# Optimization experiments

Hardware: AMD Instinct MI355X
Metric: run time of the kernel (lower is better)

Reference implementation:

```python
import jax, jax.numpy as jnp
import numpy as np

C_IN, SEQ_LEN, K, G = 12, 8192, 8, 64
DIVISOR = 2 if G > 1 else 1
_G = G // DIVISOR
MAX_EXP = int(np.log2((SEQ_LEN - 1) / (9 - 1)))
DILATIONS = [2 ** e for e in range(MAX_EXP + 1)]   # 10 dilations for seq_len=8192
PADDINGS = [(9 - 1) * d // 2 for d in DILATIONS]
C_IN_PER = int(np.clip(C_IN // 2, 2, 8))
BATCH = 32


def _normalize(W):
    # zero-mean, L1-normalized over the kernel taps (last dim)
    W = W - W.mean(-1, keepdims=True)
    return W / jnp.abs(W).sum(-1, keepdims=True)


def setup_inputs() -> dict:
    key = jax.random.key(0)
    kx, kw, ki = jax.random.split(key, 3)
    X = jax.random.normal(kx, (BATCH, C_IN, SEQ_LEN), dtype=jnp.float32)
    # W: (num_dilations, divisor, k*_g, 1, 9) grouped-conv kernels
    W = _normalize(jax.random.normal(kw, (len(DILATIONS), DIVISOR, K * _G, 1, 9), dtype=jnp.float32))
    # I: (num_dilations, divisor, _g, c_in_per) channel-gather indices
    I = jax.random.randint(ki, (len(DILATIONS), DIVISOR, _G, C_IN_PER), 0, C_IN)
    return {"X": X, "W": W, "I": I}


def _branch(inp, Wd, d, p):
    # inp: (bs, _G, L); Wd: (K*_G, 1, 9); grouped dilated conv, 1 in-ch -> K out-ch per group
    z = jax.lax.conv_general_dilated(
        inp, Wd, window_strides=(1,), padding=[(p, p)], rhs_dilation=(d,),
        dimension_numbers=("NCH", "OIH", "NCH"), feature_group_count=_G)
    bs = inp.shape[0]
    z = z.reshape(bs, _G, K, -1)                      # (bs, _G, K, L)
    max_vals = z.max(axis=2)                          # (bs, _G, L)
    max_idx = z.argmax(axis=2)
    min_idx = z.argmin(axis=2)
    # histogram over K bins: sum of max values at argmax bin; count at argmin bin
    cmax = jnp.stack([jnp.where(max_idx == i, max_vals, 0.0).sum(-1) for i in range(K)], axis=-1)
    cmin = jnp.stack([(min_idx == i).astype(inp.dtype).sum(-1) for i in range(K)], axis=-1)
    return cmax, cmin                                 # each (bs, _G, K)


def reference(X, W, I):
    diff_X = jnp.diff(X, axis=-1)
    Z = []
    for di, (d, p) in enumerate(zip(DILATIONS, PADDINGS)):
        for j in range(min(2, G)):
            src = X if j == 0 else diff_X
            inp = src[:, I[di, j]].sum(2)             # gather channels, sum -> (bs, _G, L)
            cmax, cmin = _branch(inp, W[di, j], d, p)
            Z.append(cmax)
            Z.append(cmin)
    Z = jnp.concatenate(Z, axis=1)                    # (bs, 4*num_dilations*_G, K)
    return jax.nn.relu(Z)
```

## Files before the change

kernel.cpp:

```cpp
#include <hip/hip_runtime.h>


typedef __fp16 h2_t __attribute__((ext_vector_type(2)));

#define NB    32
#define CIN   12
#define SEQ   8192
#define NG    32
#define CPER  6
#define OUTCH 1280
#define XS_FLOATS 7728
#define GRID  10240

template <int DI>
__device__ __forceinline__ void hydra_body(
    const float* __restrict__ X, const float* __restrict__ W,
    const int* __restrict__ I, float* __restrict__ out,
    float* Xs, float* Smx, int j, int b, int chunk) {

  constexpr int d   = 1 << DI;
  constexpr int R   = (d < 16) ? d : 16;
  constexpr int rb  = (DI < 4) ? DI : 4;
  constexpr int Mm  = SEQ / d;
  constexpr int TMc = 512 / R;
  constexpr int TM  = (TMc < Mm) ? TMc : Mm;
  constexpr int MC  = Mm / TM;
  constexpr int RC  = d / R;
  constexpr int NR  = (RC * MC) / 16;
  constexpr int SR  = TM + 8;
  constexpr int CS  = R * SR + 4;
  constexpr int CL  = (R >= 8) ? TM : (TM * R / 8);
  constexpr int REP = (R == 16) ? 2 : 1;

  const int L = SEQ - j;
  const int tid = threadIdx.x;
  const int g = tid >> 3, s = tid & 7;

  h2_t Wp[8][4];
  float Wt[8];
  {
    const float* wp = W + (size_t)((DI * 2 + j) * 256 + g * 8) * 9;
#pragma unroll
    for (int k = 0; k < 8; ++k) {
#pragma unroll
      for (int t = 0; t < 4; ++t)
        Wp[k][t] = __builtin_amdgcn_cvt_pkrtz(wp[k * 9 + 2 * t], wp[k * 9 + 2 * t + 1]);
      Wt[k] = wp[k * 9 + 8];
    }
  }
  const float* base[CPER];
  {
    const int* ip = I + ((DI * 2 + j) * NG + g) * CPER;
#pragma unroll
    for (int i = 0; i < CPER; ++i) base[i] = Xs + ip[i] * CS;
  }

#pragma unroll
  for (int k = 0; k < 8; ++k) Smx[k * 256 + tid] = 0.f;

  unsigned long long cmnp = 0ull;

  for (int n = 0; n < NR; ++n) {
    const int cidx = chunk + 16 * n;
    const int rc = cidx & (RC - 1);
    const int mc = cidx / RC;
    const int r0 = rc * R;
    const int m0 = mc * TM;

    if (NR > 1 && n) __syncthreads();

    {
      const float* xb0 = X + (size_t)b * CIN * SEQ;
      if (j == 0) {
        for (int f = tid; f < R * SR; f += 256) {
          int rr = f & (R - 1), mm = f >> rb, mp = m0 + mm - 4;
          int pos = r0 + rr + mp * d;
          bool ok = (mp >= 0) && (pos < L);
          int lo = rr * SR + mm;
          const float* xp = xb0 + pos;
#pragma unroll
          for (int ch = 0; ch < CIN; ++ch) {
            Xs[ch * CS + lo] = ok ? xp[0] : 0.f;
            xp += SEQ;
          }
        }
      } else {
        for (int f = tid; f < R * SR; f += 256) {
          int rr = f & (R - 1), mm = f >> rb, mp = m0 + mm - 4;
          int pos = r0 + rr + mp * d;
          bool ok = (mp >= 0) && (pos < L);
          int lo = rr * SR + mm;
          const float* xp = xb0 + pos;
#pragma unroll
          for (int ch = 0; ch < CIN; ++ch) {
            Xs[ch * CS + lo] = ok ? (xp[1] - xp[0]) : 0.f;
            xp += SEQ;
          }
        }
      }
    }
    __syncthreads();

#pragma unroll
    for (int rep = 0; rep < REP; ++rep) {
      int rr = (R == 16) ? (s + (rep << 3)) : (s & (R - 1));
      int mst = (R >= 8) ? 0 : ((s >> rb) * CL);
      int rowoff = rr * SR + mst;

      auto ldsum = [&](int idx) {
        float4 r = *reinterpret_cast<const float4*>(base[0] + idx);
#pragma unroll
        for (int i = 1; i < CPER; ++i) {
          float4 t = *reinterpret_cast<const float4*>(base[i] + idx);
          r.x += t.x; r.y += t.y; r.z += t.z; r.w += t.w;
        }
        return r;
      };

      float4 w0 = ldsum(rowoff);
      float4 w1 = ldsum(rowoff + 4);
#pragma unroll 1
      for (int st = 0; st < CL; st += 4) {
        float4 w2 = ldsum(rowoff + st + 8);
        float xv[12] = {w0.x, w0.y, w0.z, w0.w,
                        w1.x, w1.y, w1.z, w1.w,
                        w2.x, w2.y, w2.z, w2.w};
        h2_t E[5], O[5];
#pragma unroll
        for (int i = 0; i < 5; ++i) {
          E[i] = __builtin_amdgcn_cvt_pkrtz(xv[2 * i],     xv[2 * i + 1]);
          O[i] = __builtin_amdgcn_cvt_pkrtz(xv[2 * i + 1], xv[2 * i + 2]);
        }
#pragma unroll
        for (int p = 0; p < 4; ++p) {
          const h2_t* P = (p & 1) ? (O + (p >> 1)) : (E + (p >> 1));
          float tail = xv[8 + p];
          float zp[8];
#pragma unroll
          for (int k = 0; k < 8; ++k) {
            float acc = Wt[k] * tail;
            acc = __builtin_amdgcn_fdot2(Wp[k][3], P[3], acc, false);
            acc = __builtin_amdgcn_fdot2(Wp[k][2], P[2], acc, false);
            acc = __builtin_amdgcn_fdot2(Wp[k][1], P[1], acc, false);
            acc = __builtin_amdgcn_fdot2(Wp[k][0], P[0], acc, false);
            zp[k] = __uint_as_float((__float_as_uint(acc) & 0xFFFFFFF8u) | (unsigned)k);
          }
          float mxp = fmaxf(fmaxf(fmaxf(zp[0], zp[1]), fmaxf(zp[2], zp[3])),
                            fmaxf(fmaxf(zp[4], zp[5]), fmaxf(zp[6], zp[7])));
          float mnp = fminf(fminf(fminf(zp[0], zp[1]), fminf(zp[2], zp[3])),
                            fminf(fminf(zp[4], zp[5]), fminf(zp[6], zp[7])));
          unsigned mxb = __float_as_uint(mxp);
          Smx[((mxb & 7u) << 8) + tid] += mxp;
          unsigned mnb = __float_as_uint(mnp);
          cmnp += 1ull << ((mnb & 7u) << 3);
        }
        w0 = w1; w1 = w2;
      }
    }
  }

  __syncthreads();

  {
    int cbase = (DI * 2 + j) * 64;
    float sum = 0.f;
#pragma unroll
    for (int s2 = 0; s2 < 8; ++s2) sum += Smx[(s << 8) + (g << 3) + s2];
    atomicAdd(out + ((size_t)b * OUTCH + cbase + g) * 8 + s, sum);

    int cnts[8];
#pragma unroll
    for (int k = 0; k < 8; ++k) cnts[k] = (int)((cmnp >> (k * 8)) & 0xFFull);
#pragma unroll
    for (int k = 0; k < 8; ++k) {
#pragma unroll
      for (int off = 1; off < 8; off <<= 1)
        cnts[k] += __shfl_xor(cnts[k], off);
    }
    int vn = cnts[0];
#pragma unroll
    for (int k = 1; k < 8; ++k) vn = (s == k) ? cnts[k] : vn;
    atomicAdd(out + ((size_t)b * OUTCH + cbase + 32 + g) * 8 + s, (float)vn);
  }
}

__global__ __launch_bounds__(256, 3) void hydra_fused(
    const float* __restrict__ X, const float* __restrict__ W,
    const int* __restrict__ I, float* __restrict__ out) {
  __shared__ float Xs[XS_FLOATS];
  __shared__ float Smx[2048];
  int u = blockIdx.x;
  int dj = u % 20;
  int rest = u / 20;
  int b = rest & 31;
  int chunk = rest >> 5;
  int j = dj & 1;
  switch (dj >> 1) {
    case 0: hydra_body<0>(X, W, I, out, Xs, Smx, j, b, chunk); break;
    case 1: hydra_body<1>(X, W, I, out, Xs, Smx, j, b, chunk); break;
    case 2: hydra_body<2>(X, W, I, out, Xs, Smx, j, b, chunk); break;
    case 3: hydra_body<3>(X, W, I, out, Xs, Smx, j, b, chunk); break;
    case 4: hydra_body<4>(X, W, I, out, Xs, Smx, j, b, chunk); break;
    case 5: hydra_body<5>(X, W, I, out, Xs, Smx, j, b, chunk); break;
    case 6: hydra_body<6>(X, W, I, out, Xs, Smx, j, b, chunk); break;
    case 7: hydra_body<7>(X, W, I, out, Xs, Smx, j, b, chunk); break;
    case 8: hydra_body<8>(X, W, I, out, Xs, Smx, j, b, chunk); break;
    case 9: hydra_body<9>(X, W, I, out, Xs, Smx, j, b, chunk); break;
  }
}

__global__ void hydra_relu(float* __restrict__ out, int n) {
  int i = blockIdx.x * 256 + threadIdx.x;
  if (i < n) out[i] = fmaxf(out[i], 0.f);
}

extern "C" void kernel_launch(void* const* d_in, const int* in_sizes, int n_in,
                              void* d_out, int out_size, void* d_ws, size_t ws_size,
                              hipStream_t stream) {
  const float* X = (const float*)d_in[0];
  const float* W = (const float*)d_in[1];
  const int*   I = (const int*)d_in[2];
  float* out = (float*)d_out;

  (void)hipMemsetAsync(d_out, 0, (size_t)out_size * sizeof(float), stream);
  hydra_fused<<<GRID, 256, 0, stream>>>(X, W, I, out);
  hydra_relu<<<(out_size + 255) / 256, 256, 0, stream>>>(out, out_size);
}
```

Baseline: 428.3 us.

## Stage inputs as fp16 in LDS and sum channels with packed half adds

Result: slower. 453.9 us (+6.0%).

```diff
diff --git a/kernel.cpp b/kernel.cpp
--- a/kernel.cpp
+++ b/kernel.cpp
@@ -2,6 +2,7 @@
 
 
 typedef __fp16 h2_t __attribute__((ext_vector_type(2)));
+typedef _Float16 f16x8 __attribute__((ext_vector_type(8)));
 
 #define NB    32
 #define CIN   12
@@ -9,14 +10,14 @@
 #define NG    32
 #define CPER  6
 #define OUTCH 1280
-#define XS_FLOATS 7728
+#define XS_HALVES 9312
 #define GRID  10240
 
 template <int DI>
 __device__ __forceinline__ void hydra_body(
     const float* __restrict__ X, const float* __restrict__ W,
     const int* __restrict__ I, float* __restrict__ out,
-    float* Xs, float* Smx, int j, int b, int chunk) {
+    _Float16* Xs, float* Smx, int j, int b, int chunk) {
 
   constexpr int d   = 1 << DI;
   constexpr int R   = (d < 16) ? d : 16;
@@ -27,8 +28,8 @@
   constexpr int MC  = Mm / TM;
   constexpr int RC  = d / R;
   constexpr int NR  = (RC * MC) / 16;
-  constexpr int SR  = TM + 8;
-  constexpr int CS  = R * SR + 4;
+  constexpr int SR  = TM + 16;
+  constexpr int CS  = R * SR + 8;
   constexpr int CL  = (R >= 8) ? TM : (TM * R / 8);
   constexpr int REP = (R == 16) ? 2 : 1;
 
@@ -36,8 +37,7 @@
   const int tid = threadIdx.x;
   const int g = tid >> 3, s = tid & 7;
 
-  h2_t Wp[8][4];
-  float Wt[8];
+  h2_t Wp[8][5];
   {
     const float* wp = W + (size_t)((DI * 2 + j) * 256 + g * 8) * 9;
 #pragma unroll
@@ -45,10 +45,10 @@
 #pragma unroll
       for (int t = 0; t < 4; ++t)
         Wp[k][t] = __builtin_amdgcn_cvt_pkrtz(wp[k * 9 + 2 * t], wp[k * 9 + 2 * t + 1]);
-      Wt[k] = wp[k * 9 + 8];
-    }
-  }
-  const float* base[CPER];
+      Wp[k][4] = __builtin_amdgcn_cvt_pkrtz(wp[k * 9 + 8], 0.f);
+    }
+  }
+  const _Float16* base[CPER];
   {
     const int* ip = I + ((DI * 2 + j) * NG + g) * CPER;
 #pragma unroll
@@ -75,12 +75,12 @@
         for (int f = tid; f < R * SR; f += 256) {
           int rr = f & (R - 1), mm = f >> rb, mp = m0 + mm - 4;
           int pos = r0 + rr + mp * d;
-          bool ok = (mp >= 0) && (pos < L);
+          bool ok = (mp >= 0) && (mm < TM + 8) && (pos < L);
           int lo = rr * SR + mm;
           const float* xp = xb0 + pos;
 #pragma unroll
           for (int ch = 0; ch < CIN; ++ch) {
-            Xs[ch * CS + lo] = ok ? xp[0] : 0.f;
+            Xs[ch * CS + lo] = ok ? (_Float16)xp[0] : (_Float16)0.f;
             xp += SEQ;
           }
         }
@@ -88,12 +88,12 @@
         for (int f = tid; f < R * SR; f += 256) {
           int rr = f & (R - 1), mm = f >> rb, mp = m0 + mm - 4;
           int pos = r0 + rr + mp * d;
-          bool ok = (mp >= 0) && (pos < L);
+          bool ok = (mp >= 0) && (mm < TM + 8) && (pos < L);
           int lo = rr * SR + mm;
           const float* xp = xb0 + pos;
 #pragma unroll
           for (int ch = 0; ch < CIN; ++ch) {
-            Xs[ch * CS + lo] = ok ? (xp[1] - xp[0]) : 0.f;
+            Xs[ch * CS + lo] = ok ? (_Float16)(xp[1] - xp[0]) : (_Float16)0.f;
             xp += SEQ;
           }
         }
@@ -107,42 +107,50 @@
       int mst = (R >= 8) ? 0 : ((s >> rb) * CL);
       int rowoff = rr * SR + mst;
 
-      auto ldsum = [&](int idx) {
-        float4 r = *reinterpret_cast<const float4*>(base[0] + idx);
-#pragma unroll
-        for (int i = 1; i < CPER; ++i) {
-          float4 t = *reinterpret_cast<const float4*>(base[i] + idx);
-          r.x += t.x; r.y += t.y; r.z += t.z; r.w += t.w;
-        }
+      auto sum8 = [&](int idx) {
+        f16x8 r = *reinterpret_cast<const f16x8*>(base[0] + idx);
+#pragma unroll
+        for (int i = 1; i < CPER; ++i)
+          r = r + *reinterpret_cast<const f16x8*>(base[i] + idx);
         return r;
       };
 
-      float4 w0 = ldsum(rowoff);
-      float4 w1 = ldsum(rowoff + 4);
+      f16x8 a = sum8(rowoff);
+      f16x8 bw = sum8(rowoff + 8);
 #pragma unroll 1
-      for (int st = 0; st < CL; st += 4) {
-        float4 w2 = ldsum(rowoff + st + 8);
-        float xv[12] = {w0.x, w0.y, w0.z, w0.w,
-                        w1.x, w1.y, w1.z, w1.w,
-                        w2.x, w2.y, w2.z, w2.w};
-        h2_t E[5], O[5];
-#pragma unroll
-        for (int i = 0; i < 5; ++i) {
-          E[i] = __builtin_amdgcn_cvt_pkrtz(xv[2 * i],     xv[2 * i + 1]);
-          O[i] = __builtin_amdgcn_cvt_pkrtz(xv[2 * i + 1], xv[2 * i + 2]);
-        }
-#pragma unroll
-        for (int p = 0; p < 4; ++p) {
-          const h2_t* P = (p & 1) ? (O + (p >> 1)) : (E + (p >> 1));
-          float tail = xv[8 + p];
+      for (int st = 0; st < CL; st += 8) {
+        f16x8 nb = sum8(rowoff + st + 16);
+        int wv[9];
+        {
+          int4 ai = __builtin_bit_cast(int4, a);
+          int4 bi = __builtin_bit_cast(int4, bw);
+          wv[0] = ai.x; wv[1] = ai.y; wv[2] = ai.z; wv[3] = ai.w;
+          wv[4] = bi.x; wv[5] = bi.y; wv[6] = bi.z; wv[7] = bi.w;
+          wv[8] = ai.x;
+        }
+        h2_t E[8], O[8];
+#pragma unroll
+        for (int i = 0; i < 8; ++i) {
+          E[i] = __builtin_bit_cast(h2_t, wv[i]);
+          O[i] = __builtin_bit_cast(h2_t,
+                   (int)__builtin_amdgcn_alignbit((unsigned)wv[i + 1],
+                                                  (unsigned)wv[i], 16));
+        }
+#pragma unroll
+        for (int p = 0; p < 8; ++p) {
+          h2_t pr[5];
+#pragma unroll
+          for (int t = 0; t < 5; ++t)
+            pr[t] = (p & 1) ? O[((p - 1) >> 1) + t] : E[(p >> 1) + t];
           float zp[8];
 #pragma unroll
           for (int k = 0; k < 8; ++k) {
-            float acc = Wt[k] * tail;
-            acc = __builtin_amdgcn_fdot2(Wp[k][3], P[3], acc, false);
-            acc = __builtin_amdgcn_fdot2(Wp[k][2], P[2], acc, false);
-            acc = __builtin_amdgcn_fdot2(Wp[k][1], P[1], acc, false);
-            acc = __builtin_amdgcn_fdot2(Wp[k][0], P[0], acc, false);
+            float acc = 0.f;
+            acc = __builtin_amdgcn_fdot2(Wp[k][4], pr[4], acc, false);
+            acc = __builtin_amdgcn_fdot2(Wp[k][3], pr[3], acc, false);
+            acc = __builtin_amdgcn_fdot2(Wp[k][2], pr[2], acc, false);
+            acc = __builtin_amdgcn_fdot2(Wp[k][1], pr[1], acc, false);
+            acc = __builtin_amdgcn_fdot2(Wp[k][0], pr[0], acc, false);
             zp[k] = __uint_as_float((__float_as_uint(acc) & 0xFFFFFFF8u) | (unsigned)k);
           }
           float mxp = fmaxf(fmaxf(fmaxf(zp[0], zp[1]), fmaxf(zp[2], zp[3])),
@@ -154,7 +162,7 @@
           unsigned mnb = __float_as_uint(mnp);
           cmnp += 1ull << ((mnb & 7u) << 3);
         }
-        w0 = w1; w1 = w2;
+        a = bw; bw = nb;
       }
     }
   }
@@ -187,7 +195,7 @@
 __global__ __launch_bounds__(256, 3) void hydra_fused(
     const float* __restrict__ X, const float* __restrict__ W,
     const int* __restrict__ I, float* __restrict__ out) {
-  __shared__ float Xs[XS_FLOATS];
+  __shared__ _Float16 Xs[XS_HALVES];
   __shared__ float Smx[2048];
   int u = blockIdx.x;
   int dj = u % 20;
```
